# Performance work log

Hardware: AMD Instinct MI355X
Metric: run time of the kernel (lower is better)

The kernel has to match this reference:

```python
import jax, jax.numpy as jnp
import numpy as np

IMG = 224
PS = 2
C_IN = 3
EMBED = 768
BATCH = 256
SLICES = IMG // 2            # 112
L = 2 * (SLICES // PS)       # 112 levels
K = IMG * PS                 # 448 gathered (a,b) pairs per level
D_IN = K * C_IN              # 1344


def _build_levels(n=IMG, slices=SLICES, ps=PS):
    """Replicates LUnraveling index construction (natural order; set() in the
    original only permutes within a level, which is equivalent up to a fixed
    permutation of weight columns for random init)."""
    a_list, b_list = [], []
    ar = np.arange(n)
    for i in range(slices // ps):
        cols = range(i * ps, (i + 1) * ps)
        # 'up' level: pairs (j, col) for j in range(n), concatenated over ps cols
        a_list.append(np.concatenate([ar for _ in cols]))
        b_list.append(np.concatenate([np.full(n, c) for c in cols]))
        # 'right' level: pairs (n - slices + col, j) for j in range(n)
        a_list.append(np.concatenate([np.full(n, n - slices + c) for c in cols]))
        b_list.append(np.concatenate([ar for _ in cols]))
    return (np.stack(a_list).astype(np.int32), np.stack(b_list).astype(np.int32))


def setup_inputs() -> dict:
    key = jax.random.key(0)
    k1, k2, k3 = jax.random.split(key, 3)
    x = jax.random.normal(k1, (BATCH, C_IN, IMG, IMG), dtype=jnp.float32)
    W = jax.random.normal(k2, (EMBED, D_IN), dtype=jnp.float32) * (1.0 / np.sqrt(D_IN))
    b = jax.random.normal(k3, (EMBED,), dtype=jnp.float32) * 0.01
    a_np, b_np = _build_levels()
    return {"x": x, "W": W, "b": b,
            "a_idx": jnp.asarray(a_np), "b_idx": jnp.asarray(b_np)}


def reference(x, W, b, a_idx, b_idx):
    B = x.shape[0]
    # gather: x[:, :, a, b] with (L,K) index arrays -> (B, C, L, K)
    g = x[:, :, a_idx, b_idx]
    # per-level flatten(1) in torch flattens (C, K) C-major -> (B, L, C*K)
    g = jnp.transpose(g, (0, 2, 1, 3)).reshape(B, L, C_IN * K)
    # shared linear projection per level token
    tokens = jnp.einsum('bld,ed->ble', g, W) + b
    return tokens  # (B, L, EMBED); norm is Identity (norm_layer=None)
```

## Files before the change

### kernel.cpp

```cpp
#include <hip/hip_runtime.h>
#include <stdint.h>


#define IMG   224
#define NLEV  112
#define CIN   3
#define DIN   1344
#define EMB   768
#define BATCH 256
#define MTOT  28672
#define NT    21
#define GBM   256
#define GBN   128

#define BM    128
#define BN    128
#define BK    64
#define LDP   72

#define AS1 __attribute__((address_space(1)))
#define AS3 __attribute__((address_space(3)))

typedef __attribute__((ext_vector_type(8))) short   short8;
typedef __attribute__((ext_vector_type(4))) float   floatx4;

__device__ __forceinline__ unsigned short f2bf(float f) {
    unsigned u = __float_as_uint(f);
    unsigned r = (u + 0x7fffu + ((u >> 16) & 1u)) >> 16;
    return (unsigned short)r;
}
__device__ __forceinline__ float bf2f(unsigned short s) {
    return __uint_as_float(((unsigned)s) << 16);
}
__device__ __forceinline__ unsigned pack2(float a, float b) {
    return (unsigned)f2bf(a) | ((unsigned)f2bf(b) << 16);
}

__global__ void detect_dtype(const unsigned short* __restrict__ W, int* flag) {
    __shared__ int s;
    if (threadIdx.x == 0) s = 0;
    __syncthreads();
    int bad = 0;
    for (int k = threadIdx.x; k < 4096; k += 256) {
        unsigned v = (unsigned)W[2 * k] & 0x7FFFu;
        if (v >= 0x4000u) bad = 1;
    }
    if (bad) atomicOr(&s, 1);
    __syncthreads();
    if (threadIdx.x == 0) *flag = s;
}

__global__ __launch_bounds__(256)
void pack_all(const void* __restrict__ Xv, const void* __restrict__ Wv,
              const void* __restrict__ Bv,
              unsigned short* __restrict__ Gc, unsigned short* __restrict__ Wb,
              float* __restrict__ Bf, int* __restrict__ flagOut,
              int b0, int chb, int doW)
{
    __shared__ __align__(16) unsigned short lds[IMG * 128];
    __shared__ int sflag;

    const int tid = threadIdx.x;

    {
        if (tid == 0) sflag = 0;
        int bad = 0;
        const unsigned short* Wu = (const unsigned short*)Wv;
        #pragma unroll
        for (int k = tid; k < 512; k += 256) {
            unsigned v = (unsigned)Wu[2 * k] & 0x7FFFu;
            if (v >= 0x4000u) bad = 1;
        }
        __syncthreads();
        if (bad) atomicOr(&sflag, 1);
        __syncthreads();
    }
    const bool F32 = (sflag != 0);

    if (blockIdx.x == 0 && blockIdx.y == 0 && tid == 0)
        *flagOut = F32 ? 1 : 0;

    if (blockIdx.y == 3) {
        if (!doW) return;
        if (F32) {
            const int total = EMB * DIN / 8;
            for (int idx = blockIdx.x * 256 + tid; idx < total; idx += chb * 256) {
                const float4* s = (const float4*)((const float*)Wv + (size_t)idx * 8);
                float4 x0 = s[0], x1 = s[1];
                uint4 o;
                o.x = pack2(x0.x, x0.y); o.y = pack2(x0.z, x0.w);
                o.z = pack2(x1.x, x1.y); o.w = pack2(x1.z, x1.w);
                ((uint4*)Wb)[idx] = o;
            }
        }
        if (blockIdx.x == 0) {
            for (int e = tid; e < EMB; e += 256)
                Bf[e] = F32 ? ((const float*)Bv)[e]
                            : bf2f(((const unsigned short*)Bv)[e]);
        }
        return;
    }

    const int bl = blockIdx.x;
    const int c  = blockIdx.y;
    const size_t plane = ((size_t)(b0 + bl) * CIN + c) * (size_t)(IMG * IMG);
    unsigned short* Grow = Gc + (size_t)bl * NLEV * DIN + (size_t)c * 448;

    if (F32) {
        const float* src = (const float*)Xv + plane + (size_t)NLEV * IMG;
        for (int v = tid; v < 3136; v += 256) {
            const int i  = v / 56;
            const int kk = (v - i * 56) * 8;
            const float4* s = (const float4*)(src + (size_t)v * 8);
            float4 x0 = s[0], x1 = s[1];
            uint4 o;
            o.x = pack2(x0.x, x0.y); o.y = pack2(x0.z, x0.w);
            o.z = pack2(x1.x, x1.y); o.w = pack2(x1.z, x1.w);
            *(uint4*)(Grow + (size_t)(2 * i + 1) * DIN + kk) = o;
        }
    }

    for (int v = tid; v < 3136; v += 256) {
        const int r  = v / 14;
        const int vv = v - r * 14;
        const int key = (r >> 3) & 15;
        uint2 o0, o1;
        if (F32) {
            const float4* s = (const float4*)((const float*)Xv + plane
                              + (size_t)r * IMG + (size_t)vv * 8);
            float4 x0 = s[0], x1 = s[1];
            o0.x = pack2(x0.x, x0.y); o0.y = pack2(x0.z, x0.w);
            o1.x = pack2(x1.x, x1.y); o1.y = pack2(x1.z, x1.w);
        } else {
            const uint2* s = (const uint2*)((const unsigned short*)Xv + plane
                              + (size_t)r * IMG + (size_t)vv * 8);
            o0 = s[0]; o1 = s[1];
        }
        *(uint2*)&lds[r * 128 + ((2 * vv)     ^ key) * 4] = o0;
        *(uint2*)&lds[r * 128 + ((2 * vv + 1) ^ key) * 4] = o1;
    }
    __syncthreads();

    for (int idx = tid; idx < 56 * 56; idx += 256) {
        const int pr   = idx / 56;
        const int j    = idx - pr * 56;
        const int half = j / 28;
        const int r0   = (j - half * 28) * 8;
        const int qb   = pr >> 1;
        const int sh   = (pr & 1) * 2;
        unsigned short h[8];
        #pragma unroll
        for (int m = 0; m < 8; m++) {
            const int r = r0 + m;
            const unsigned v = *(const unsigned*)
                &lds[r * 128 + (qb ^ ((r >> 3) & 15)) * 4 + sh];
            h[m] = half ? (unsigned short)(v >> 16) : (unsigned short)(v & 0xFFFFu);
        }
        uint4 o;
        o.x = (unsigned)h[0] | ((unsigned)h[1] << 16);
        o.y = (unsigned)h[2] | ((unsigned)h[3] << 16);
        o.z = (unsigned)h[4] | ((unsigned)h[5] << 16);
        o.w = (unsigned)h[6] | ((unsigned)h[7] << 16);
        *(uint4*)(Grow + (size_t)(2 * pr) * DIN + half * IMG + r0) = o;
    }
}

__global__ __launch_bounds__(512)
void gemm_packed(const unsigned short* __restrict__ G,
                 const unsigned short* __restrict__ Xu,
                 const unsigned short* __restrict__ Wraw,
                 const unsigned short* __restrict__ Wb,
                 const float* __restrict__ Bf,
                 float* __restrict__ Out,
                 const int* __restrict__ flag,
                 int b0)
{
    __shared__ __align__(16) unsigned short As[2][GBM * 64];
    __shared__ __align__(16) unsigned short Bs[2][GBN * 64];

    const int tid  = threadIdx.x;
    const int wave = tid >> 6;
    const int lane = tid & 63;
    const bool useX = (*flag == 0);

    const int bid = blockIdx.x;
    const int nwg = gridDim.x;
    const int q = nwg >> 3, r = nwg & 7;
    const int xcd = bid & 7, s = bid >> 3;
    const int lid = (xcd < r ? xcd * (q + 1) : r * (q + 1) + (xcd - r) * q) + s;
    const int mT = lid / 6;
    const int nT = lid - mT * 6;
    const int mBase = mT * GBM;
    const int nBase = nT * GBN;

    const int wm   = wave >> 1, wn = wave & 1;
    const int lrow = lane & 15;
    const int kq   = (lane >> 4) << 3;
    const int swz  = (lrow & 7) << 3;

    const unsigned short* Wsrc = useX ? Wraw : Wb;

    floatx4 acc[4][4];
    #pragma unroll
    for (int i = 0; i < 4; i++)
        #pragma unroll
        for (int j = 0; j < 4; j++)
            acc[i][j] = (floatx4){0.f, 0.f, 0.f, 0.f};

    const unsigned short* aP[4];
    int aExtra[4];
    unsigned aOff[4];
    #pragma unroll
    for (int i = 0; i < 4; i++) {
        const int idx = (i * 8 + wave) * 64 + lane;
        const int row = idx >> 3, k8 = idx & 7;
        const int jc  = k8 ^ (row & 7);
        const int m   = mBase + row;
        const int b   = m / NLEV;
        const int l   = m - b * NLEV;
        if ((l & 1) && useX) {
            aP[i] = Xu + (size_t)(b0 + b) * (CIN * IMG * IMG)
                       + (size_t)(111 + l) * IMG + jc * 8;
            aExtra[i] = 49728;
        } else {
            aP[i] = G + (size_t)m * DIN + jc * 8;
            aExtra[i] = 0;
        }
        aOff[i] = (unsigned)((i * 8 + wave) * 512);
    }
    const unsigned short* bP[2];
    unsigned bOff[2];
    #pragma unroll
    for (int i = 0; i < 2; i++) {
        const int idx = (i * 8 + wave) * 64 + lane;
        const int row = idx >> 3, k8 = idx & 7;
        const int jc  = k8 ^ (row & 7);
        bP[i] = Wsrc + (size_t)(nBase + row) * DIN + jc * 8;
        bOff[i] = (unsigned)((i * 8 + wave) * 512);
    }

    #pragma unroll
    for (int i = 0; i < 4; i++)
        __builtin_amdgcn_global_load_lds((const AS1 void*)(aP[i]),
                                         (AS3 void*)(&As[0][0] + aOff[i]), 16, 0, 0);
    #pragma unroll
    for (int i = 0; i < 2; i++)
        __builtin_amdgcn_global_load_lds((const AS1 void*)(bP[i]),
                                         (AS3 void*)(&Bs[0][0] + bOff[i]), 16, 0, 0);

    int cur = 0;
    for (int t = 0; t < NT; ++t) {
        if (t < NT - 1) {
            const int kt = (t + 1) * 64;
            const int c  = kt / 448;
            #pragma unroll
            for (int i = 0; i < 4; i++)
                __builtin_amdgcn_global_load_lds(
                    (const AS1 void*)(aP[i] + kt + c * aExtra[i]),
                    (AS3 void*)(&As[cur ^ 1][0] + aOff[i]), 16, 0, 0);
            #pragma unroll
            for (int i = 0; i < 2; i++)
                __builtin_amdgcn_global_load_lds(
                    (const AS1 void*)(bP[i] + kt),
                    (AS3 void*)(&Bs[cur ^ 1][0] + bOff[i]), 16, 0, 0);
            asm volatile("s_waitcnt vmcnt(6)" ::: "memory");
        } else {
            asm volatile("s_waitcnt vmcnt(0)" ::: "memory");
        }
        __builtin_amdgcn_s_barrier();
        __builtin_amdgcn_sched_barrier(0);

        const unsigned short* Ab = &As[cur][0];
        const unsigned short* Bb = &Bs[cur][0];
        #pragma unroll
        for (int k0 = 0; k0 < 64; k0 += 32) {
            short8 af[4], bfv[4];
            #pragma unroll
            for (int mi = 0; mi < 4; mi++)
                af[mi] = *(const short8*)&Ab[(wm * 64 + mi * 16 + lrow) * 64
                                             + ((k0 + kq) ^ swz)];
            #pragma unroll
            for (int ni = 0; ni < 4; ni++)
                bfv[ni] = *(const short8*)&Bb[(wn * 64 + ni * 16 + lrow) * 64
                                              + ((k0 + kq) ^ swz)];
            __builtin_amdgcn_s_setprio(1);
            #pragma unroll
            for (int mi = 0; mi < 4; mi++)
                #pragma unroll
                for (int ni = 0; ni < 4; ni++)
                    acc[mi][ni] = __builtin_amdgcn_mfma_f32_16x16x32_bf16(
                        af[mi], bfv[ni], acc[mi][ni], 0, 0, 0);
            __builtin_amdgcn_s_setprio(0);
        }
        __builtin_amdgcn_s_barrier();
        __builtin_amdgcn_sched_barrier(0);
        cur ^= 1;
    }

    const int quad = lane >> 4;
    #pragma unroll
    for (int ni = 0; ni < 4; ni++) {
        const int col = nBase + wn * 64 + ni * 16 + lrow;
        const float bv = Bf[col];
        #pragma unroll
        for (int mi = 0; mi < 4; mi++) {
            const int rbase = mBase + wm * 64 + mi * 16 + quad * 4;
            floatx4 a = acc[mi][ni];
            Out[(size_t)(rbase + 0) * EMB + col] = a[0] + bv;
            Out[(size_t)(rbase + 1) * EMB + col] = a[1] + bv;
            Out[(size_t)(rbase + 2) * EMB + col] = a[2] + bv;
            Out[(size_t)(rbase + 3) * EMB + col] = a[3] + bv;
        }
    }
}

template<bool F32>
__global__ __launch_bounds__(256, 2)
void lfreq_fused_gemm(const void* __restrict__ Xv,
                      const void* __restrict__ Wv,
                      const void* __restrict__ Bv,
                      const int* __restrict__ Aidx,
                      const int* __restrict__ Bidx,
                      float* __restrict__ Out,
                      const int* __restrict__ flag)
{
    if (*flag != (F32 ? 1 : 0)) return;

    __shared__ __align__(16) unsigned short As[BM][LDP];
    __shared__ __align__(16) unsigned short Bs[BN][LDP];

    const int tid   = threadIdx.x;
    const int wave  = tid >> 6;
    const int lane  = tid & 63;
    const int mBase = blockIdx.x * BM;
    const int nBase = blockIdx.y * BN;

    const int srow  = tid >> 1;
    const int shalf = tid & 1;
    const int am = mBase + srow;
    const int bb = am / NLEV;
    const int ll = am - bb * NLEV;

    floatx4 acc[4][4];
    #pragma unroll
    for (int i = 0; i < 4; i++)
        #pragma unroll
        for (int jj = 0; jj < 4; jj++)
            acc[i][jj] = (floatx4){0.f, 0.f, 0.f, 0.f};

    const int wm   = wave >> 1;
    const int wn   = wave & 1;
    const int lrow = lane & 15;
    const int kq   = (lane >> 4) << 3;

    for (int kt = 0; kt < DIN; kt += BK) {
        {
            const int koff = kt + shalf * 32;
            uint4* dst = (uint4*)&Bs[srow][shalf * 32];
            if (F32) {
                const float4* g = (const float4*)((const float*)Wv
                                + (size_t)(nBase + srow) * DIN + koff);
                #pragma unroll
                for (int q = 0; q < 4; q++) {
                    float4 v0 = g[2*q], v1 = g[2*q+1];
                    uint4 o;
                    o.x = pack2(v0.x, v0.y); o.y = pack2(v0.z, v0.w);
                    o.z = pack2(v1.x, v1.y); o.w = pack2(v1.z, v1.w);
                    dst[q] = o;
                }
            } else {
                const uint4* g = (const uint4*)((const unsigned short*)Wv
                               + (size_t)(nBase + srow) * DIN + koff);
                #pragma unroll
                for (int q = 0; q < 4; q++) dst[q] = g[q];
            }
        }
        {
            const int d0  = kt + shalf * 32;
            const int c   = (d0 >= 896) ? 2 : (d0 >= 448 ? 1 : 0);
            const int kk0 = d0 - c * 448;
            const int4* ap = (const int4*)(Aidx + ll * 448 + kk0);
            const int4* bp = (const int4*)(Bidx + ll * 448 + kk0);
            unsigned* du = (unsigned*)&As[srow][shalf * 32];
            if (F32) {
                const float* plane = (const float*)Xv
                    + (size_t)bb * (CIN * IMG * IMG) + (size_t)c * (IMG * IMG);
                #pragma unroll
                for (int q = 0; q < 8; q++) {
                    int4 av = ap[q], bv = bp[q];
                    du[2*q+0] = pack2(plane[av.x * IMG + bv.x], plane[av.y * IMG + bv.y]);
                    du[2*q+1] = pack2(plane[av.z * IMG + bv.z], plane[av.w * IMG + bv.w]);
                }
            } else {
                const unsigned short* plane = (const unsigned short*)Xv
                    + (size_t)bb * (CIN * IMG * IMG) + (size_t)c * (IMG * IMG);
                #pragma unroll
                for (int q = 0; q < 8; q++) {
                    int4 av = ap[q], bv = bp[q];
                    unsigned e0 = plane[av.x * IMG + bv.x];
                    unsigned e1 = plane[av.y * IMG + bv.y];
                    unsigned e2 = plane[av.z * IMG + bv.z];
                    unsigned e3 = plane[av.w * IMG + bv.w];
                    du[2*q+0] = e0 | (e1 << 16);
                    du[2*q+1] = e2 | (e3 << 16);
                }
            }
        }
        __syncthreads();

        #pragma unroll
        for (int k0 = 0; k0 < BK; k0 += 32) {
            short8 af[4], bfv[4];
            #pragma unroll
            for (int mi = 0; mi < 4; mi++)
                af[mi] = *(const short8*)&As[wm*64 + mi*16 + lrow][k0 + kq];
            #pragma unroll
            for (int ni = 0; ni < 4; ni++)
                bfv[ni] = *(const short8*)&Bs[wn*64 + ni*16 + lrow][k0 + kq];
            #pragma unroll
            for (int mi = 0; mi < 4; mi++)
                #pragma unroll
                for (int ni = 0; ni < 4; ni++)
                    acc[mi][ni] = __builtin_amdgcn_mfma_f32_16x16x32_bf16(
                        af[mi], bfv[ni], acc[mi][ni], 0, 0, 0);
        }
        __syncthreads();
    }

    const int quad = lane >> 4;
    #pragma unroll
    for (int ni = 0; ni < 4; ni++) {
        const int col = nBase + wn*64 + ni*16 + lrow;
        const float bv = F32 ? ((const float*)Bv)[col]
                             : bf2f(((const unsigned short*)Bv)[col]);
        #pragma unroll
        for (int mi = 0; mi < 4; mi++) {
            const int rbase = mBase + wm*64 + mi*16 + quad*4;
            floatx4 a = acc[mi][ni];
            Out[(size_t)(rbase+0)*EMB + col] = a[0] + bv;
            Out[(size_t)(rbase+1)*EMB + col] = a[1] + bv;
            Out[(size_t)(rbase+2)*EMB + col] = a[2] + bv;
            Out[(size_t)(rbase+3)*EMB + col] = a[3] + bv;
        }
    }
}

extern "C" void kernel_launch(void* const* d_in, const int* in_sizes, int n_in,
                              void* d_out, int out_size, void* d_ws, size_t ws_size,
                              hipStream_t stream) {
    const void* X    = d_in[0];
    const void* Wt   = d_in[1];
    const void* Bias = d_in[2];
    const int*  Ai   = (const int*)d_in[3];
    const int*  Bi   = (const int*)d_in[4];
    float* Out = (float*)d_out;

    char* ws  = (char*)d_ws;
    int* flag = (int*)ws;

    float* Bf          = (float*)(ws + 256);
    unsigned short* Wb = (unsigned short*)(ws + 4096);
    const size_t gOff  = 4096 + (size_t)EMB * DIN * 2;
    unsigned short* Gc = (unsigned short*)(ws + gOff);

    int CHB = 0;
    const int cand[5] = {256, 128, 64, 32, 16};
    for (int t = 0; t < 5; t++) {
        if (gOff + (size_t)cand[t] * NLEV * DIN * 2 <= ws_size) { CHB = cand[t]; break; }
    }

    if (CHB == 0) {
        detect_dtype<<<dim3(1), dim3(256), 0, stream>>>((const unsigned short*)Wt, flag);
        dim3 grid(MTOT / BM, EMB / BN);
        lfreq_fused_gemm<false><<<grid, dim3(256), 0, stream>>>(X, Wt, Bias, Ai, Bi, Out, flag);
        lfreq_fused_gemm<true ><<<grid, dim3(256), 0, stream>>>(X, Wt, Bias, Ai, Bi, Out, flag);
        return;
    }

    for (int b0 = 0; b0 < BATCH; b0 += CHB) {
        dim3 pgrid(CHB, 4);
        pack_all<<<pgrid, dim3(256), 0, stream>>>(X, Wt, Bias, Gc, Wb, Bf, flag,
                                                  b0, CHB, b0 == 0 ? 1 : 0);
        dim3 ggrid(CHB * NLEV / GBM * 6);
        gemm_packed<<<ggrid, dim3(512), 0, stream>>>(
            Gc, (const unsigned short*)X, (const unsigned short*)Wt, Wb, Bf,
            Out + (size_t)b0 * NLEV * EMB, flag, b0);
    }
}
```

Before: 354.8 us.

## Shrink GEMM tile to 128x128 with single-buffered LDS and 256 threads

Changes the packed GEMM from a 256x128 tile with 8 waves and double-buffered LDS prefetch to a 128x128 tile with 4 waves, a single LDS buffer and plain __syncthreads between load and compute. This cuts LDS use and doubles the number of workgroups, which may raise occupancy and improve load balance across CUs. In exchange it drops the overlap of global loads with MFMA work, the wave priority hints and the larger tile's data reuse. It also adds a chunk size of 8 to the workspace fallback list.

After: 344.1 us. 3.0% less time.

```diff
diff --git a/kernel.cpp b/kernel.cpp
--- a/kernel.cpp
+++ b/kernel.cpp
@@ -10,8 +10,6 @@
 #define BATCH 256
 #define MTOT  28672
 #define NT    21
-#define GBM   256
-#define GBN   128
 
 #define BM    128
 #define BN    128
@@ -165,7 +163,7 @@
     }
 }
 
-__global__ __launch_bounds__(512)
+__global__ __launch_bounds__(256)
 void gemm_packed(const unsigned short* __restrict__ G,
                  const unsigned short* __restrict__ Xu,
                  const unsigned short* __restrict__ Wraw,
@@ -175,8 +173,8 @@
                  const int* __restrict__ flag,
                  int b0)
 {
-    __shared__ __align__(16) unsigned short As[2][GBM * 64];
-    __shared__ __align__(16) unsigned short Bs[2][GBN * 64];
+    __shared__ __align__(16) unsigned short As[128 * 64];
+    __shared__ __align__(16) unsigned short Bs[128 * 64];
 
     const int tid  = threadIdx.x;
     const int wave = tid >> 6;
@@ -190,8 +188,8 @@
     const int lid = (xcd < r ? xcd * (q + 1) : r * (q + 1) + (xcd - r) * q) + s;
     const int mT = lid / 6;
     const int nT = lid - mT * 6;
-    const int mBase = mT * GBM;
-    const int nBase = nT * GBN;
+    const int mBase = mT * 128;
+    const int nBase = nT * 128;
 
     const int wm   = wave >> 1, wn = wave & 1;
     const int lrow = lane & 15;
@@ -212,7 +210,7 @@
     unsigned aOff[4];
     #pragma unroll
     for (int i = 0; i < 4; i++) {
-        const int idx = (i * 8 + wave) * 64 + lane;
+        const int idx = (i * 4 + wave) * 64 + lane;
         const int row = idx >> 3, k8 = idx & 7;
         const int jc  = k8 ^ (row & 7);
         const int m   = mBase + row;
@@ -226,75 +224,52 @@
             aP[i] = G + (size_t)m * DIN + jc * 8;
             aExtra[i] = 0;
         }
-        aOff[i] = (unsigned)((i * 8 + wave) * 512);
-    }
-    const unsigned short* bP[2];
-    unsigned bOff[2];
-    #pragma unroll
-    for (int i = 0; i < 2; i++) {
-        const int idx = (i * 8 + wave) * 64 + lane;
+        aOff[i] = (unsigned)((i * 4 + wave) * 512);
+    }
+    const unsigned short* bP[4];
+    unsigned bOff[4];
+    #pragma unroll
+    for (int i = 0; i < 4; i++) {
+        const int idx = (i * 4 + wave) * 64 + lane;
         const int row = idx >> 3, k8 = idx & 7;
         const int jc  = k8 ^ (row & 7);
         bP[i] = Wsrc + (size_t)(nBase + row) * DIN + jc * 8;
-        bOff[i] = (unsigned)((i * 8 + wave) * 512);
-    }
-
-    #pragma unroll
-    for (int i = 0; i < 4; i++)
-        __builtin_amdgcn_global_load_lds((const AS1 void*)(aP[i]),
-                                         (AS3 void*)(&As[0][0] + aOff[i]), 16, 0, 0);
-    #pragma unroll
-    for (int i = 0; i < 2; i++)
-        __builtin_amdgcn_global_load_lds((const AS1 void*)(bP[i]),
-                                         (AS3 void*)(&Bs[0][0] + bOff[i]), 16, 0, 0);
-
-    int cur = 0;
+        bOff[i] = (unsigned)((i * 4 + wave) * 512);
+    }
+
     for (int t = 0; t < NT; ++t) {
-        if (t < NT - 1) {
-            const int kt = (t + 1) * 64;
-            const int c  = kt / 448;
-            #pragma unroll
-            for (int i = 0; i < 4; i++)
-                __builtin_amdgcn_global_load_lds(
-                    (const AS1 void*)(aP[i] + kt + c * aExtra[i]),
-                    (AS3 void*)(&As[cur ^ 1][0] + aOff[i]), 16, 0, 0);
-            #pragma unroll
-            for (int i = 0; i < 2; i++)
-                __builtin_amdgcn_global_load_lds(
-                    (const AS1 void*)(bP[i] + kt),
-                    (AS3 void*)(&Bs[cur ^ 1][0] + bOff[i]), 16, 0, 0);
-            asm volatile("s_waitcnt vmcnt(6)" ::: "memory");
-        } else {
-            asm volatile("s_waitcnt vmcnt(0)" ::: "memory");
-        }
-        __builtin_amdgcn_s_barrier();
-        __builtin_amdgcn_sched_barrier(0);
-
-        const unsigned short* Ab = &As[cur][0];
-        const unsigned short* Bb = &Bs[cur][0];
+        const int kt = t * 64;
+        const int c  = kt / 448;
+        #pragma unroll
+        for (int i = 0; i < 4; i++) {
+            __builtin_amdgcn_global_load_lds(
+                (const AS1 void*)(aP[i] + kt + c * aExtra[i]),
+                (AS3 void*)(As + aOff[i]), 16, 0, 0);
+            __builtin_amdgcn_global_load_lds(
+                (const AS1 void*)(bP[i] + kt),
+                (AS3 void*)(Bs + bOff[i]), 16, 0, 0);
+        }
+        __syncthreads();
+
         #pragma unroll
         for (int k0 = 0; k0 < 64; k0 += 32) {
             short8 af[4], bfv[4];
             #pragma unroll
             for (int mi = 0; mi < 4; mi++)
-                af[mi] = *(const short8*)&Ab[(wm * 64 + mi * 16 + lrow) * 64
+                af[mi] = *(const short8*)&As[(wm * 64 + mi * 16 + lrow) * 64
                                              + ((k0 + kq) ^ swz)];
             #pragma unroll
             for (int ni = 0; ni < 4; ni++)
-                bfv[ni] = *(const short8*)&Bb[(wn * 64 + ni * 16 + lrow) * 64
+                bfv[ni] = *(const short8*)&Bs[(wn * 64 + ni * 16 + lrow) * 64
                                               + ((k0 + kq) ^ swz)];
-            __builtin_amdgcn_s_setprio(1);
             #pragma unroll
             for (int mi = 0; mi < 4; mi++)
                 #pragma unroll
                 for (int ni = 0; ni < 4; ni++)
                     acc[mi][ni] = __builtin_amdgcn_mfma_f32_16x16x32_bf16(
                         af[mi], bfv[ni], acc[mi][ni], 0, 0, 0);
-            __builtin_amdgcn_s_setprio(0);
-        }
-        __builtin_amdgcn_s_barrier();
-        __builtin_amdgcn_sched_barrier(0);
-        cur ^= 1;
+        }
+        __syncthreads();
     }
 
     const int quad = lane >> 4;
@@ -464,8 +439,8 @@
     unsigned short* Gc = (unsigned short*)(ws + gOff);
 
     int CHB = 0;
-    const int cand[5] = {256, 128, 64, 32, 16};
-    for (int t = 0; t < 5; t++) {
+    const int cand[6] = {256, 128, 64, 32, 16, 8};
+    for (int t = 0; t < 6; t++) {
         if (gOff + (size_t)cand[t] * NLEV * DIN * 2 <= ws_size) { CHB = cand[t]; break; }
     }
 
@@ -481,8 +456,8 @@
         dim3 pgrid(CHB, 4);
         pack_all<<<pgrid, dim3(256), 0, stream>>>(X, Wt, Bias, Gc, Wb, Bf, flag,
                                                   b0, CHB, b0 == 0 ? 1 : 0);
-        dim3 ggrid(CHB * NLEV / GBM * 6);
-        gemm_packed<<<ggrid, dim3(512), 0, stream>>>(
+        dim3 ggrid(CHB * NLEV / 128 * 6);
+        gemm_packed<<<ggrid, dim3(256), 0, stream>>>(
             Gc, (const unsigned short*)X, (const unsigned short*)Wt, Wb, Bf,
             Out + (size_t)b0 * NLEV * EMB, flag, b0);
     }
```
